# Kernel optimization log

Hardware: AMD Instinct MI355X
Metric: run time of the kernel (lower is better)

The kernel has to match this reference:

```python
import jax, jax.numpy as jnp
import numpy as np
from jax import lax

B, FQ, T, H = 2, 257, 100, 96
S, DIN, N, R, KF, KM = 8, 192, 16, 6, 5, 4
GROUPS = 8

def _ln(x, g, b, eps=1e-5):
    m = x.mean(-1, keepdims=True)
    v = ((x - m) ** 2).mean(-1, keepdims=True)
    return (x - m) / jnp.sqrt(v + eps) * g + b

def _silu(x):
    return x * jax.nn.sigmoid(x)

def _fconv(x, g, b, cw, cb, alpha):
    Bb, Fq, Tt, Hh = x.shape
    y = _ln(x, g, b)  # LayerNorm over hidden dim H (seq_last=True path)
    y = y.transpose(0, 2, 3, 1).reshape(Bb * Tt, Hh, Fq)
    pad = (cw.shape[-1] - 1) // 2
    y = lax.conv_general_dilated(y, cw, (1,), [(pad, pad)],
                                 feature_group_count=GROUPS,
                                 dimension_numbers=('NCH', 'OIH', 'NCH')) + cb[:, None]
    y = jnp.where(y > 0, y, alpha[:, None] * y)  # PReLU per channel
    return y.reshape(Bb, Tt, Hh, Fq).transpose(0, 3, 1, 2)

def _full(x, g, b, sq_w, sq_b, fw, fb, uw, ub):
    Bb, Fq, Tt, Hh = x.shape
    y = _ln(x, g, b).transpose(0, 2, 3, 1).reshape(Bb * Tt, Hh, Fq)
    y = _silu(jnp.einsum('bhf,sh->bsf', y, sq_w) + sq_b[:, None])   # squeeze 1x1 conv
    y = jnp.einsum('bgf,gkf->bgk', y, fw) + fb                      # grouped full-band linear
    y = _silu(jnp.einsum('bsf,hs->bhf', y, uw) + ub[:, None])       # unsqueeze 1x1 conv
    return y.reshape(Bb, Tt, Hh, Fq).transpose(0, 3, 1, 2)

def _mamba(x, in_w, cw, cb, xp_w, dt_w, dt_b, A_log, Dp, out_w):
    # x: [Bm, T, H] -> Mamba selective scan (d_inner=DIN, d_state=N, dt_rank=R)
    Bm, Tt, Hh = x.shape
    xz = x @ in_w.T                                  # [Bm,T,2*DIN]
    xin, z = xz[..., :DIN], xz[..., DIN:]
    xc = xin.transpose(0, 2, 1)                      # [Bm,DIN,T]
    xc = lax.conv_general_dilated(xc, cw, (1,), [(KM - 1, 0)],
                                  feature_group_count=DIN,
                                  dimension_numbers=('NCH', 'OIH', 'NCH')) + cb[:, None]
    xc = _silu(xc).transpose(0, 2, 1)                # [Bm,T,DIN]
    dbl = xc @ xp_w.T                                # [Bm,T,R+2N]
    dt = jax.nn.softplus(dbl[..., :R] @ dt_w.T + dt_b)
    Bs, Cs = dbl[..., R:R + N], dbl[..., R + N:R + 2 * N]
    A = -jnp.exp(A_log)                              # [DIN,N]

    def step(h, inp):
        dt_t, x_t, B_t, C_t = inp
        h = jnp.exp(dt_t[..., None] * A) * h + (dt_t * x_t)[..., None] * B_t[:, None, :]
        return h, jnp.einsum('bdn,bn->bd', h, C_t)

    h0 = jnp.zeros((Bm, DIN, N), x.dtype)
    _, ys = lax.scan(step, h0, (dt.transpose(1, 0, 2), xc.transpose(1, 0, 2),
                                Bs.transpose(1, 0, 2), Cs.transpose(1, 0, 2)))
    y = ys.transpose(1, 0, 2) + xc * Dp
    return (y * _silu(z)) @ out_w.T

def setup_inputs():
    key = jax.random.key(0)
    ks = jax.random.split(key, 32)
    n = lambda i, shape, s=0.1: jax.random.normal(ks[i], shape) * s
    inp = dict(
        x=jax.random.normal(ks[0], (B, FQ, T, H)),
        ln1_g=jnp.ones((H,)), ln1_b=jnp.zeros((H,)),
        conv1_w=n(1, (H, H // GROUPS, KF), 0.2), conv1_b=n(2, (H,)),
        prelu1_a=jnp.full((H,), 0.25),
        lnf_g=jnp.ones((H,)), lnf_b=jnp.zeros((H,)),
        sq_w=n(3, (S, H)), sq_b=n(4, (S,)),
        full_w=n(5, (S, FQ, FQ), 0.06), full_b=n(6, (S, FQ)),
        unsq_w=n(7, (H, S), 0.3), unsq_b=n(8, (H,)),
        ln2_g=jnp.ones((H,)), ln2_b=jnp.zeros((H,)),
        conv2_w=n(9, (H, H // GROUPS, KF), 0.2), conv2_b=n(10, (H,)),
        prelu2_a=jnp.full((H,), 0.25),
        lnm_g=jnp.ones((H,)), lnm_b=jnp.zeros((H,)),
    )
    for p, off in (('m0_', 11), ('m1_', 21)):
        inp[p + 'in_w'] = n(off, (2 * DIN, H))
        inp[p + 'conv_w'] = n(off + 1, (DIN, 1, KM), 0.3)
        inp[p + 'conv_b'] = n(off + 2, (DIN,))
        inp[p + 'xp_w'] = n(off + 3, (R + 2 * N, DIN))
        inp[p + 'dt_w'] = n(off + 4, (DIN, R))
        inp[p + 'dt_b'] = n(off + 5, (DIN,)) - 2.0
        inp[p + 'A_log'] = jnp.log(jax.random.uniform(ks[off + 6], (DIN, N), minval=0.5, maxval=1.5))
        inp[p + 'D'] = jnp.ones((DIN,)) + n(off + 7, (DIN,))
        inp[p + 'out_w'] = n(off + 8, (H, DIN))
    return inp

def reference(x, ln1_g, ln1_b, conv1_w, conv1_b, prelu1_a,
              lnf_g, lnf_b, sq_w, sq_b, full_w, full_b, unsq_w, unsq_b,
              ln2_g, ln2_b, conv2_w, conv2_b, prelu2_a, lnm_g, lnm_b,
              m0_in_w, m0_conv_w, m0_conv_b, m0_xp_w, m0_dt_w, m0_dt_b, m0_A_log, m0_D, m0_out_w,
              m1_in_w, m1_conv_w, m1_conv_b, m1_xp_w, m1_dt_w, m1_dt_b, m1_A_log, m1_D, m1_out_w):
    x = x + _fconv(x, ln1_g, ln1_b, conv1_w, conv1_b, prelu1_a)
    x = x + _full(x, lnf_g, lnf_b, sq_w, sq_b, full_w, full_b, unsq_w, unsq_b)
    x = x + _fconv(x, ln2_g, ln2_b, conv2_w, conv2_b, prelu2_a)
    Bb, Fq, Tt, Hh = x.shape
    xn = _ln(x, lnm_g, lnm_b)
    yf = _mamba(xn.reshape(Bb * Fq, Tt, Hh),
                m0_in_w, m0_conv_w, m0_conv_b, m0_xp_w, m0_dt_w, m0_dt_b, m0_A_log, m0_D, m0_out_w)
    yb = _mamba(jnp.flip(xn, 2).reshape(Bb * Fq, Tt, Hh),
                m1_in_w, m1_conv_w, m1_conv_b, m1_xp_w, m1_dt_w, m1_dt_b, m1_A_log, m1_D, m1_out_w)
    x_fw = x + yf.reshape(Bb, Fq, Tt, Hh)
    x_bw = jnp.flip(x, 2) + yb.reshape(Bb, Fq, Tt, Hh)
    return (x_fw + jnp.flip(x_bw, 2)) / 2
```

## Files before the change

### kernel.cpp

```cpp
#include <hip/hip_runtime.h>
#include <math.h>

constexpr int kB   = 2;
constexpr int kF   = 257;
constexpr int kT   = 100;
constexpr int kH   = 96;
constexpr int kS   = 8;
constexpr int kD   = 192;
constexpr int kN   = 16;
constexpr int kR   = 6;
constexpr int kKF  = 5;
constexpr int kKM  = 4;
constexpr int kG   = 8;
constexpr int kGC  = kH / kG;
constexpr int kBM  = kB * kF;
constexpr int kROWS = kB * kF * kT;
constexpr int kNX  = kROWS * kH;
constexpr int kNM  = kROWS * kD;
constexpr int kDBL = kR + 2 * kN;
constexpr int kDBLP = 48;

__device__ inline float wave_reduce_sum(float v) {
    for (int o = 32; o > 0; o >>= 1) v += __shfl_xor(v, o, 64);
    return v;
}
__device__ inline float silu_f(float x) { return x / (1.f + __expf(-x)); }
__device__ inline float softplus_f(float x) { return x > 20.f ? x : log1pf(__expf(x)); }

__global__ void ln_kernel(const float* __restrict__ in, float* __restrict__ out,
                          const float* __restrict__ g, const float* __restrict__ b,
                          int rows) {
    int wave = threadIdx.x >> 6;
    int lane = threadIdx.x & 63;
    int r = blockIdx.x * 4 + wave;
    if (r >= rows) return;
    const float* p = in + (size_t)r * kH;
    float v0 = p[lane];
    float v1 = (lane < 32) ? p[64 + lane] : 0.f;
    float s = wave_reduce_sum(v0 + v1);
    float mean = s * (1.f / 96.f);
    float d0 = v0 - mean;
    float d1 = (lane < 32) ? (v1 - mean) : 0.f;
    float vs = wave_reduce_sum(d0 * d0 + d1 * d1);
    float rstd = rsqrtf(vs * (1.f / 96.f) + 1e-5f);
    float* q = out + (size_t)r * kH;
    q[lane] = d0 * rstd * g[lane] + b[lane];
    if (lane < 32) q[64 + lane] = d1 * rstd * g[64 + lane] + b[64 + lane];
}

#define FDOT(S,K) \
  acc += xw[S][0].x*wr[K][0] + xw[S][0].y*wr[K][1] + xw[S][0].z*wr[K][2] + xw[S][0].w*wr[K][3] \
       + xw[S][1].x*wr[K][4] + xw[S][1].y*wr[K][5] + xw[S][1].z*wr[K][6] + xw[S][1].w*wr[K][7] \
       + xw[S][2].x*wr[K][8] + xw[S][2].y*wr[K][9] + xw[S][2].z*wr[K][10]+ xw[S][2].w*wr[K][11];

#define FSTEP(S0,S1,S2,S3,S4)                                              \
  if (f < fmax) {                                                          \
    const float4* cp = (const float4*)(Xs + (f + 4) * 12);                 \
    xw[S4][0] = cp[0]; xw[S4][1] = cp[1]; xw[S4][2] = cp[2];               \
    float acc = bias;                                                      \
    FDOT(S0,0) FDOT(S1,1) FDOT(S2,2) FDOT(S3,3) FDOT(S4,4)                 \
    float yv = acc > 0.f ? acc : alpha_h * acc;                            \
    size_t oi = ((size_t)(bb * kF + f) * kT + tt) * kH + g12 + hh;         \
    out[oi] = resid[oi] + yv;                                              \
    f++;                                                                   \
  }

__global__ __launch_bounds__(256)
void fconv_kernel(const float* __restrict__ ln, const float* __restrict__ resid,
                  float* __restrict__ out, const float* __restrict__ w,
                  const float* __restrict__ cb, const float* __restrict__ alpha) {
    __shared__ float Xs[261 * 12];
    __shared__ float Ws[kGC * kKF * 12];
    int g = blockIdx.x, tt = blockIdx.y, bb = blockIdx.z;
    int g12 = g * 12;
    int tid = threadIdx.x;

    for (int i = tid; i < 720; i += 256) Ws[i] = w[g * 720 + i];
    for (int i = tid; i < 257 * 12; i += 256) {
        int fs = i / 12, ci = i - fs * 12;
        Xs[(fs + 2) * 12 + ci] = ln[((size_t)(bb * kF + fs) * kT + tt) * kH + g12 + ci];
    }
    if (tid < 48) {
        const int padr[4] = {0, 1, 259, 260};
        Xs[padr[tid / 12] * 12 + (tid % 12)] = 0.f;
    }
    __syncthreads();

    int lane = tid & 63, wave = tid >> 6;
    int hh = lane % 12, fi = lane / 12;
    if (fi >= 5) return;
    int slot = wave * 5 + fi;
    int f0 = slot * 13;
    int fmax = min(f0 + 13, kF);

    float wr[5][12];
    #pragma unroll
    for (int k = 0; k < 5; k++)
        #pragma unroll
        for (int ci = 0; ci < 12; ci++)
            wr[k][ci] = Ws[hh * 60 + ci * 5 + k];

    float bias = cb[g12 + hh];
    float alpha_h = alpha[g12 + hh];

    float4 xw[5][3];
    #pragma unroll
    for (int s = 0; s < 4; s++) {
        int row = min(f0 + s, 260);
        const float4* cp = (const float4*)(Xs + row * 12);
        xw[s][0] = cp[0]; xw[s][1] = cp[1]; xw[s][2] = cp[2];
    }
    int f = f0;
    for (int rep = 0; rep < 3; rep++) {
        FSTEP(0,1,2,3,4)
        FSTEP(1,2,3,4,0)
        FSTEP(2,3,4,0,1)
        FSTEP(3,4,0,1,2)
        FSTEP(4,0,1,2,3)
    }
}

__global__ void squeeze_kernel(const float* __restrict__ ln, float* __restrict__ s1,
                               const float* __restrict__ sqw, const float* __restrict__ sqb) {
    int bt = blockIdx.x;
    int f = blockIdx.y * 64 + threadIdx.x;
    if (f >= kF) return;
    int b = bt / kT, t = bt % kT;
    const float* row = ln + ((size_t)(b * kF + f) * kT + t) * kH;
    float acc[kS];
    for (int s = 0; s < kS; s++) acc[s] = 0.f;
    for (int h = 0; h < kH; h++) {
        float v = row[h];
        for (int s = 0; s < kS; s++) acc[s] += v * sqw[s * kH + h];
    }
    for (int s = 0; s < kS; s++)
        s1[((size_t)bt * kS + s) * kF + f] = silu_f(acc[s] + sqb[s]);
}

__global__ __launch_bounds__(256)
void fullmat_gemm(const float* __restrict__ s1, float* __restrict__ s2,
                  const float* __restrict__ fw, const float* __restrict__ fb) {
    __shared__ float As[64 * 64];
    __shared__ float Bs[64 * 64];
    int k0 = blockIdx.x * 64, bt0 = blockIdx.y * 64, g = blockIdx.z;
    int tid = threadIdx.x;
    int rt = tid >> 4, ct = tid & 15;
    float acc[4][4];
    #pragma unroll
    for (int i = 0; i < 4; i++)
        #pragma unroll
        for (int j = 0; j < 4; j++) acc[i][j] = 0.f;

    for (int f0 = 0; f0 < kF; f0 += 64) {
        int fcnt = min(64, kF - f0);
        for (int i = tid; i < 64 * 64; i += 256) {
            int m = i & 63, fk = i >> 6;
            int bt = bt0 + m, f = f0 + fk;
            As[fk * 64 + m] = (bt < kB * kT && f < kF)
                ? s1[((size_t)bt * kS + g) * kF + f] : 0.f;
            int k = k0 + m;
            Bs[fk * 64 + m] = (k < kF && f < kF)
                ? fw[(size_t)g * kF * kF + (size_t)k * kF + f] : 0.f;
        }
        __syncthreads();
        for (int f = 0; f < fcnt; f++) {
            float4 a4 = *(const float4*)&As[f * 64 + rt * 4];
            float4 b4 = *(const float4*)&Bs[f * 64 + ct * 4];
            float ar[4] = {a4.x, a4.y, a4.z, a4.w};
            float br[4] = {b4.x, b4.y, b4.z, b4.w};
            #pragma unroll
            for (int i = 0; i < 4; i++)
                #pragma unroll
                for (int j = 0; j < 4; j++) acc[i][j] += ar[i] * br[j];
        }
        __syncthreads();
    }
    #pragma unroll
    for (int i = 0; i < 4; i++) {
        int bt = bt0 + rt * 4 + i;
        if (bt >= kB * kT) continue;
        #pragma unroll
        for (int j = 0; j < 4; j++) {
            int k = k0 + ct * 4 + j;
            if (k >= kF) continue;
            s2[((size_t)bt * kS + g) * kF + k] = acc[i][j] + fb[g * kF + k];
        }
    }
}

__global__ void unsqueeze_kernel(const float* __restrict__ s2, float* __restrict__ x,
                                 const float* __restrict__ uw, const float* __restrict__ ub) {
    int idx = blockIdx.x * blockDim.x + threadIdx.x;
    if (idx >= kNX) return;
    int h = idx % kH;
    int t = (idx / kH) % kT;
    int f = (idx / (kH * kT)) % kF;
    int b = idx / (kH * kT * kF);
    int bt = b * kT + t;
    float acc = ub[h];
    for (int s = 0; s < kS; s++)
        acc += s2[((size_t)bt * kS + s) * kF + f] * uw[h * kS + s];
    x[idx] += silu_f(acc);
}

__global__ void transpose_kernel(const float* __restrict__ in, float* __restrict__ out,
                                 int rows, int cols) {
    int idx = blockIdx.x * blockDim.x + threadIdx.x;
    if (idx >= rows * cols) return;
    int r = idx / cols, c = idx % cols;
    out[c * rows + r] = in[idx];
}

__global__ void xppad_kernel(const float* __restrict__ w, float* __restrict__ wp) {
    int i = blockIdx.x * 256 + threadIdx.x;
    if (i >= kD * kDBLP) return;
    int d = i / kDBLP, n = i % kDBLP;
    wp[i] = (n < kDBL) ? w[n * kD + d] : 0.f;
}

__global__ __launch_bounds__(256)
void inproj_gemm(const float* __restrict__ xn, const float* __restrict__ wT,
                 float* __restrict__ xin, float* __restrict__ z) {
    __shared__ float Al[64 * 96];
    int r0 = blockIdx.x * 64;
    int c0 = blockIdx.y * 128;
    int tid = threadIdx.x;
    for (int i = tid; i < 64 * 24; i += 256) {
        int rr = i / 24, cq = i - rr * 24;
        int r = r0 + rr; if (r >= kROWS) r = kROWS - 1;
        *(float4*)&Al[rr * 96 + cq * 4] = *(const float4*)&xn[(size_t)r * kH + cq * 4];
    }
    __syncthreads();
    int rt = tid >> 5, ct = tid & 31;
    const float* ap = Al + rt * 8 * 96;
    const float* bp = wT + c0 + ct * 4;
    float4 acc[8];
    #pragma unroll
    for (int i = 0; i < 8; i++) acc[i] = make_float4(0.f, 0.f, 0.f, 0.f);
    for (int h = 0; h < 96; h++) {
        float4 b = *(const float4*)&bp[(size_t)h * 384];
        #pragma unroll
        for (int i = 0; i < 8; i++) {
            float av = ap[i * 96 + h];
            acc[i].x += av * b.x; acc[i].y += av * b.y;
            acc[i].z += av * b.z; acc[i].w += av * b.w;
        }
    }
    int cbase = c0 + ct * 4;
    #pragma unroll
    for (int i = 0; i < 8; i++) {
        int r = r0 + rt * 8 + i;
        if (r >= kROWS) break;
        if (cbase < kD) *(float4*)&xin[(size_t)r * kD + cbase] = acc[i];
        else            *(float4*)&z[(size_t)r * kD + cbase - kD] = acc[i];
    }
}

__global__ __launch_bounds__(256)
void outproj_gemm(const float* __restrict__ ym, const float* __restrict__ zg,
                  const float* __restrict__ wpT,
                  const float* __restrict__ xres, float* __restrict__ out, int dir) {
    __shared__ float Al[64 * 192];
    int r0 = blockIdx.x * 64;
    int tid = threadIdx.x;
    for (int i = tid; i < 64 * 48; i += 256) {
        int rr = i / 48, cq = i - rr * 48;
        int r = r0 + rr; if (r >= kROWS) r = kROWS - 1;
        size_t gidx = (size_t)r * kD + cq * 4;
        float4 a = *(const float4*)&ym[gidx];
        float4 g4 = *(const float4*)&zg[gidx];
        a.x *= silu_f(g4.x); a.y *= silu_f(g4.y);
        a.z *= silu_f(g4.z); a.w *= silu_f(g4.w);
        *(float4*)&Al[rr * 192 + cq * 4] = a;
    }
    __syncthreads();
    int rt = tid >> 5, ct = tid & 31;
    const float* ap = Al + rt * 8 * 192;
    const float* bp = wpT + ct * 3;
    float acc[8][3];
    #pragma unroll
    for (int i = 0; i < 8; i++) { acc[i][0] = 0.f; acc[i][1] = 0.f; acc[i][2] = 0.f; }
    for (int h = 0; h < 192; h++) {
        float b0 = bp[h * 96], b1 = bp[h * 96 + 1], b2 = bp[h * 96 + 2];
        #pragma unroll
        for (int i = 0; i < 8; i++) {
            float av = ap[i * 192 + h];
            acc[i][0] += av * b0; acc[i][1] += av * b1; acc[i][2] += av * b2;
        }
    }
    int cbase = ct * 3;
    #pragma unroll
    for (int i = 0; i < 8; i++) {
        int r = r0 + rt * 8 + i;
        if (r >= kROWS) break;
        size_t o = (size_t)r * kH + cbase;
        #pragma unroll
        for (int j = 0; j < 3; j++) {
            float base = dir ? out[o + j] : xres[o + j];
            out[o + j] = base + 0.5f * acc[i][j];
        }
    }
}

__global__ void mconv_kernel(const float* __restrict__ xin, float* __restrict__ xc,
                             const float* __restrict__ cw, const float* __restrict__ cb, int dir) {
    int qid = blockIdx.x * blockDim.x + threadIdx.x;
    if (qid >= kROWS * 48) return;
    int r = qid / 48, d4 = (qid - r * 48) * 4;
    int bm = r / kT, t = r - bm * kT;
    float4 acc = make_float4(cb[d4], cb[d4 + 1], cb[d4 + 2], cb[d4 + 3]);
    #pragma unroll
    for (int k = 0; k < kKM; k++) {
        int ts = dir ? (t + 3 - k) : (t + k - 3);
        if (ts < 0 || ts >= kT) continue;
        float4 v = *(const float4*)&xin[((size_t)bm * kT + ts) * kD + d4];
        acc.x += v.x * cw[(d4 + 0) * kKM + k];
        acc.y += v.y * cw[(d4 + 1) * kKM + k];
        acc.z += v.z * cw[(d4 + 2) * kKM + k];
        acc.w += v.w * cw[(d4 + 3) * kKM + k];
    }
    float4 o = make_float4(silu_f(acc.x), silu_f(acc.y), silu_f(acc.z), silu_f(acc.w));
    *(float4*)&xc[(size_t)r * kD + d4] = o;
}

__global__ __launch_bounds__(256)
void xpproj_gemm(const float* __restrict__ xc, float* __restrict__ dbl,
                 const float* __restrict__ wpx) {
    __shared__ float Al[64 * 192];
    int r0 = blockIdx.x * 64;
    int tid = threadIdx.x;
    for (int i = tid; i < 64 * 48; i += 256) {
        int rr = i / 48, cq = i - rr * 48;
        int r = r0 + rr; if (r >= kROWS) r = kROWS - 1;
        *(float4*)&Al[rr * 192 + cq * 4] = *(const float4*)&xc[(size_t)r * kD + cq * 4];
    }
    __syncthreads();
    int rt = tid >> 5, ct = tid & 31;
    if (ct >= 24) return;
    const float* ap = Al + rt * 8 * 192;
    const float* bp = wpx + ct * 2;
    float acc[8][2];
    #pragma unroll
    for (int i = 0; i < 8; i++) { acc[i][0] = 0.f; acc[i][1] = 0.f; }
    for (int h = 0; h < 192; h++) {
        float b0 = bp[h * kDBLP], b1 = bp[h * kDBLP + 1];
        #pragma unroll
        for (int i = 0; i < 8; i++) {
            float av = ap[i * 192 + h];
            acc[i][0] += av * b0; acc[i][1] += av * b1;
        }
    }
    int cbase = ct * 2;
    #pragma unroll
    for (int i = 0; i < 8; i++) {
        int r = r0 + rt * 8 + i;
        if (r >= kROWS) break;
        #pragma unroll
        for (int j = 0; j < 2; j++) {
            int c = cbase + j;
            if (c < kDBL) dbl[(size_t)r * kDBL + c] = acc[i][j];
        }
    }
}

__global__ __launch_bounds__(192)
void scan2_kernel(const float* __restrict__ dbl0, const float* __restrict__ dbl1,
                  float* __restrict__ xc0, float* __restrict__ xc1,
                  const float* __restrict__ Al0, const float* __restrict__ Al1,
                  const float* __restrict__ dtw0, const float* __restrict__ dtw1,
                  const float* __restrict__ dtb0, const float* __restrict__ dtb1,
                  const float* __restrict__ Dp0, const float* __restrict__ Dp1,
                  int dirbase) {
    __shared__ float dsg[kT * 40];
    int dd = blockIdx.y;
    int dir = dirbase + dd;
    const float* dbl   = dd ? dbl1 : dbl0;
    float* xcy         = dd ? xc1  : xc0;
    const float* A_log = dd ? Al1  : Al0;
    const float* dtw   = dd ? dtw1 : dtw0;
    const float* dtb   = dd ? dtb1 : dtb0;
    const float* Dp    = dd ? Dp1  : Dp0;

    int bm = blockIdx.x;
    int d = threadIdx.x;

    const float* drow = dbl + (size_t)bm * kT * kDBL;
    for (int i = d; i < kT * kDBL; i += 192) {
        int t = i / kDBL, j = i - t * kDBL;
        int slot = (j < 6) ? j : (j + 2);
        dsg[t * 40 + slot] = drow[i];
    }
    __syncthreads();

    float A[kN], h[kN], dw[kR];
    #pragma unroll
    for (int n = 0; n < kN; n++) { A[n] = -__expf(A_log[d * kN + n]); h[n] = 0.f; }
    #pragma unroll
    for (int j = 0; j < kR; j++) dw[j] = dtw[d * kR + j];
    float db = dtb[d], Dv = Dp[d];

    float* xrow = xcy + (size_t)bm * kT * kD + d;

    for (int tb = 0; tb < kT; tb += 4) {
        int ts[4];
        float xv[4];
        #pragma unroll
        for (int u = 0; u < 4; u++) {
            ts[u] = dir ? (kT - 1 - (tb + u)) : (tb + u);
            xv[u] = xrow[(size_t)ts[u] * kD];
        }
        #pragma unroll
        for (int u = 0; u < 4; u++) {
            const float* row = dsg + ts[u] * 40;
            float4 q0 = *(const float4*)(row);
            float4 q1 = *(const float4*)(row + 4);
            float s = db + q0.x * dw[0] + q0.y * dw[1] + q0.z * dw[2]
                         + q0.w * dw[3] + q1.x * dw[4] + q1.y * dw[5];
            float dt = softplus_f(s);
            float dtx = dt * xv[u];
            float4 B0 = *(const float4*)(row + 8);
            float4 B1 = *(const float4*)(row + 12);
            float4 B2 = *(const float4*)(row + 16);
            float4 B3 = *(const float4*)(row + 20);
            float4 C0 = *(const float4*)(row + 24);
            float4 C1 = *(const float4*)(row + 28);
            float4 C2 = *(const float4*)(row + 32);
            float4 C3 = *(const float4*)(row + 36);
            float y = 0.f;
            h[0]  = __expf(dt * A[0])  * h[0]  + dtx * B0.x;  y += h[0]  * C0.x;
            h[1]  = __expf(dt * A[1])  * h[1]  + dtx * B0.y;  y += h[1]  * C0.y;
            h[2]  = __expf(dt * A[2])  * h[2]  + dtx * B0.z;  y += h[2]  * C0.z;
            h[3]  = __expf(dt * A[3])  * h[3]  + dtx * B0.w;  y += h[3]  * C0.w;
            h[4]  = __expf(dt * A[4])  * h[4]  + dtx * B1.x;  y += h[4]  * C1.x;
            h[5]  = __expf(dt * A[5])  * h[5]  + dtx * B1.y;  y += h[5]  * C1.y;
            h[6]  = __expf(dt * A[6])  * h[6]  + dtx * B1.z;  y += h[6]  * C1.z;
            h[7]  = __expf(dt * A[7])  * h[7]  + dtx * B1.w;  y += h[7]  * C1.w;
            h[8]  = __expf(dt * A[8])  * h[8]  + dtx * B2.x;  y += h[8]  * C2.x;
            h[9]  = __expf(dt * A[9])  * h[9]  + dtx * B2.y;  y += h[9]  * C2.y;
            h[10] = __expf(dt * A[10]) * h[10] + dtx * B2.z;  y += h[10] * C2.z;
            h[11] = __expf(dt * A[11]) * h[11] + dtx * B2.w;  y += h[11] * C2.w;
            h[12] = __expf(dt * A[12]) * h[12] + dtx * B3.x;  y += h[12] * C3.x;
            h[13] = __expf(dt * A[13]) * h[13] + dtx * B3.y;  y += h[13] * C3.y;
            h[14] = __expf(dt * A[14]) * h[14] + dtx * B3.z;  y += h[14] * C3.z;
            h[15] = __expf(dt * A[15]) * h[15] + dtx * B3.w;  y += h[15] * C3.w;
            xrow[(size_t)ts[u] * kD] = y + xv[u] * Dv;
        }
    }
}

extern "C" void kernel_launch(void* const* d_in, const int* in_sizes, int n_in,
                              void* d_out, int out_size, void* d_ws, size_t ws_size,
                              hipStream_t stream) {
    const float* x       = (const float*)d_in[0];
    const float* ln1_g   = (const float*)d_in[1];
    const float* ln1_b   = (const float*)d_in[2];
    const float* conv1_w = (const float*)d_in[3];
    const float* conv1_b = (const float*)d_in[4];
    const float* prelu1  = (const float*)d_in[5];
    const float* lnf_g   = (const float*)d_in[6];
    const float* lnf_b   = (const float*)d_in[7];
    const float* sq_w    = (const float*)d_in[8];
    const float* sq_b    = (const float*)d_in[9];
    const float* full_w  = (const float*)d_in[10];
    const float* full_b  = (const float*)d_in[11];
    const float* unsq_w  = (const float*)d_in[12];
    const float* unsq_b  = (const float*)d_in[13];
    const float* ln2_g   = (const float*)d_in[14];
    const float* ln2_b   = (const float*)d_in[15];
    const float* conv2_w = (const float*)d_in[16];
    const float* conv2_b = (const float*)d_in[17];
    const float* prelu2  = (const float*)d_in[18];
    const float* lnm_g   = (const float*)d_in[19];
    const float* lnm_b   = (const float*)d_in[20];

    float* ws   = (float*)d_ws;
    float* xbuf = ws;
    float* xn   = ws + (size_t)kNX;
    float* R1   = xn + (size_t)kNX;
    float* R2   = R1 + (size_t)kNM;
    float* R3   = R2 + (size_t)kNM;
    float* wTs  = R3 + (size_t)kNM;
    float* in_wT[2]  = { wTs, wTs + 2 * kD * kH };
    float* out_wp[2] = { wTs + 2 * (2 * kD * kH),
                         wTs + 2 * (2 * kD * kH) + kD * kH };
    float* xp_wp[2]  = { wTs + 2 * (2 * kD * kH) + 2 * kD * kH,
                         wTs + 2 * (2 * kD * kH) + 2 * kD * kH + kD * kDBLP };
    float* wEnd = wTs + 2 * (2 * kD * kH) + 2 * kD * kH + 2 * kD * kDBLP;
    float* R4 = wEnd;
    float* R5 = R4 + (size_t)kNM;
    size_t need_batched = (size_t)((R5 + (size_t)kNM) - ws) * sizeof(float);
    bool batched = (ws_size >= need_batched);

    const float* mw[2][8];
    for (int dir = 0; dir < 2; dir++) {
        int wi = 21 + dir * 9;
        mw[dir][0] = (const float*)d_in[wi + 1];
        mw[dir][1] = (const float*)d_in[wi + 2];
        mw[dir][2] = (const float*)d_in[wi + 4];
        mw[dir][3] = (const float*)d_in[wi + 5];
        mw[dir][4] = (const float*)d_in[wi + 6];
        mw[dir][5] = (const float*)d_in[wi + 7];
        transpose_kernel<<<(2 * kD * kH + 255) / 256, 256, 0, stream>>>(
            (const float*)d_in[wi + 0], in_wT[dir], 2 * kD, kH);
        transpose_kernel<<<(kH * kD + 255) / 256, 256, 0, stream>>>(
            (const float*)d_in[wi + 8], out_wp[dir], kH, kD);
        xppad_kernel<<<(kD * kDBLP + 255) / 256, 256, 0, stream>>>(
            (const float*)d_in[wi + 3], xp_wp[dir]);
    }

    int lnGrid = (kROWS + 3) / 4;
    int nxGrid = (kNX + 255) / 256;
    dim3 fcGrid(kG, kT, kB);
    int gemmGrid = (kROWS + 63) / 64;
    int mcGrid = (kROWS * 48 + 255) / 256;

    ln_kernel<<<lnGrid, 256, 0, stream>>>(x, R1, ln1_g, ln1_b, kROWS);
    fconv_kernel<<<fcGrid, 256, 0, stream>>>(R1, x, xbuf, conv1_w, conv1_b, prelu1);

    ln_kernel<<<lnGrid, 256, 0, stream>>>(xbuf, R1, lnf_g, lnf_b, kROWS);
    squeeze_kernel<<<dim3(kB * kT, (kF + 63) / 64), 64, 0, stream>>>(R1, R2, sq_w, sq_b);
    fullmat_gemm<<<dim3(5, 4, kS), 256, 0, stream>>>(R2, R3, full_w, full_b);
    unsqueeze_kernel<<<nxGrid, 256, 0, stream>>>(R3, xbuf, unsq_w, unsq_b);

    ln_kernel<<<lnGrid, 256, 0, stream>>>(xbuf, R1, ln2_g, ln2_b, kROWS);
    fconv_kernel<<<fcGrid, 256, 0, stream>>>(R1, xbuf, xbuf, conv2_w, conv2_b, prelu2);

    ln_kernel<<<lnGrid, 256, 0, stream>>>(xbuf, xn, lnm_g, lnm_b, kROWS);

    if (batched) {
        float* dbl0 = xn;
        float* dbl1 = xn + (size_t)kROWS * kDBL;
        inproj_gemm<<<dim3(gemmGrid, 3), 256, 0, stream>>>(xn, in_wT[0], R1, R2);
        mconv_kernel<<<mcGrid, 256, 0, stream>>>(R1, R4, mw[0][0], mw[0][1], 0);
        inproj_gemm<<<dim3(gemmGrid, 3), 256, 0, stream>>>(xn, in_wT[1], R1, R3);
        mconv_kernel<<<mcGrid, 256, 0, stream>>>(R1, R5, mw[1][0], mw[1][1], 1);
        xpproj_gemm<<<gemmGrid, 256, 0, stream>>>(R4, dbl0, xp_wp[0]);
        xpproj_gemm<<<gemmGrid, 256, 0, stream>>>(R5, dbl1, xp_wp[1]);
        scan2_kernel<<<dim3(kBM, 2), 192, 0, stream>>>(
            dbl0, dbl1, R4, R5,
            mw[0][4], mw[1][4], mw[0][2], mw[1][2],
            mw[0][3], mw[1][3], mw[0][5], mw[1][5], 0);
        outproj_gemm<<<gemmGrid, 256, 0, stream>>>(R4, R2, out_wp[0], xbuf, (float*)d_out, 0);
        outproj_gemm<<<gemmGrid, 256, 0, stream>>>(R5, R3, out_wp[1], xbuf, (float*)d_out, 1);
    } else {
        for (int dir = 0; dir < 2; dir++) {
            inproj_gemm<<<dim3(gemmGrid, 3), 256, 0, stream>>>(xn, in_wT[dir], R1, R2);
            mconv_kernel<<<mcGrid, 256, 0, stream>>>(R1, R3, mw[dir][0], mw[dir][1], dir);
            xpproj_gemm<<<gemmGrid, 256, 0, stream>>>(R3, R1, xp_wp[dir]);
            scan2_kernel<<<dim3(kBM, 1), 192, 0, stream>>>(
                R1, R1, R3, R3,
                mw[dir][4], mw[dir][4], mw[dir][2], mw[dir][2],
                mw[dir][3], mw[dir][3], mw[dir][5], mw[dir][5], dir);
            outproj_gemm<<<gemmGrid, 256, 0, stream>>>(R3, R2, out_wp[dir], xbuf, (float*)d_out, dir);
        }
    }
}
```

Measured before the change: 876.6 us.

## Fuse LayerNorm with squeeze and unsqueeze with LayerNorm; use exp2 in scan

Merges the full-band LayerNorm with the squeeze projection into one wave-per-row kernel, and merges the unsqueeze residual update with the following LayerNorm. This removes two kernel launches and several full-tensor round trips through global memory for the normalized intermediates. The selective scan now pre-scales A by log2(e) and calls exp2f instead of __expf, saving a multiply per state update. In exchange, the fused squeeze does eight wave reductions per row and writes scattered single floats from lane 0.

```diff
diff --git a/kernel.cpp b/kernel.cpp
--- a/kernel.cpp
+++ b/kernel.cpp
@@ -48,6 +48,91 @@
     if (lane < 32) q[64 + lane] = d1 * rstd * g[64 + lane] + b[64 + lane];
 }
 
+__global__ __launch_bounds__(256)
+void lnsq_kernel(const float* __restrict__ in, float* __restrict__ s1,
+                 const float* __restrict__ g, const float* __restrict__ b,
+                 const float* __restrict__ sqw, const float* __restrict__ sqb) {
+    __shared__ float sws[kS * kH];
+    int tid = threadIdx.x;
+    for (int i = tid; i < kS * kH; i += 256) sws[i] = sqw[i];
+    __syncthreads();
+    int wave = tid >> 6, lane = tid & 63;
+    int r = blockIdx.x * 4 + wave;
+    if (r >= kROWS) return;
+    int b_ = r / (kF * kT);
+    int rem = r - b_ * kF * kT;
+    int f = rem / kT;
+    int t = rem - f * kT;
+    const float* p = in + (size_t)r * kH;
+    float v0 = p[lane];
+    float v1 = (lane < 32) ? p[64 + lane] : 0.f;
+    float s = wave_reduce_sum(v0 + v1);
+    float mean = s * (1.f / 96.f);
+    float d0 = v0 - mean;
+    float d1 = (lane < 32) ? (v1 - mean) : 0.f;
+    float vs = wave_reduce_sum(d0 * d0 + d1 * d1);
+    float rstd = rsqrtf(vs * (1.f / 96.f) + 1e-5f);
+    float n0 = d0 * rstd * g[lane] + b[lane];
+    float n1 = 0.f;
+    if (lane < 32) n1 = d1 * rstd * g[64 + lane] + b[64 + lane];
+    int bt = b_ * kT + t;
+    #pragma unroll
+    for (int sq = 0; sq < kS; sq++) {
+        float part = n0 * sws[sq * kH + lane]
+                   + ((lane < 32) ? n1 * sws[sq * kH + 64 + lane] : 0.f);
+        part = wave_reduce_sum(part);
+        if (lane == 0)
+            s1[((size_t)bt * kS + sq) * kF + f] = silu_f(part + sqb[sq]);
+    }
+}
+
+__global__ __launch_bounds__(256)
+void unsq_ln_kernel(const float* __restrict__ s2, float* __restrict__ x,
+                    const float* __restrict__ uw, const float* __restrict__ ub,
+                    const float* __restrict__ g2, const float* __restrict__ b2,
+                    float* __restrict__ lnout) {
+    __shared__ float uws[kH * kS];
+    int tid = threadIdx.x;
+    for (int i = tid; i < kH * kS; i += 256) uws[i] = uw[i];
+    __syncthreads();
+    int wave = tid >> 6, lane = tid & 63;
+    int r = blockIdx.x * 4 + wave;
+    if (r >= kROWS) return;
+    int b_ = r / (kF * kT);
+    int rem = r - b_ * kF * kT;
+    int f = rem / kT;
+    int t = rem - f * kT;
+    int bt = b_ * kT + t;
+    float sv[kS];
+    #pragma unroll
+    for (int sq = 0; sq < kS; sq++)
+        sv[sq] = s2[((size_t)bt * kS + sq) * kF + f];
+    float* xr = x + (size_t)r * kH;
+    int h0 = lane, h1 = 64 + lane;
+    float acc0 = ub[h0];
+    #pragma unroll
+    for (int sq = 0; sq < kS; sq++) acc0 += sv[sq] * uws[h0 * kS + sq];
+    float x0 = xr[h0] + silu_f(acc0);
+    float x1 = 0.f;
+    if (lane < 32) {
+        float acc1 = ub[h1];
+        #pragma unroll
+        for (int sq = 0; sq < kS; sq++) acc1 += sv[sq] * uws[h1 * kS + sq];
+        x1 = xr[h1] + silu_f(acc1);
+    }
+    xr[h0] = x0;
+    if (lane < 32) xr[h1] = x1;
+    float s = wave_reduce_sum(x0 + x1);
+    float mean = s * (1.f / 96.f);
+    float d0 = x0 - mean;
+    float d1 = (lane < 32) ? (x1 - mean) : 0.f;
+    float vs = wave_reduce_sum(d0 * d0 + d1 * d1);
+    float rstd = rsqrtf(vs * (1.f / 96.f) + 1e-5f);
+    float* q = lnout + (size_t)r * kH;
+    q[h0] = d0 * rstd * g2[h0] + b2[h0];
+    if (lane < 32) q[h1] = d1 * rstd * g2[h1] + b2[h1];
+}
+
 #define FDOT(S,K) \
   acc += xw[S][0].x*wr[K][0] + xw[S][0].y*wr[K][1] + xw[S][0].z*wr[K][2] + xw[S][0].w*wr[K][3] \
        + xw[S][1].x*wr[K][4] + xw[S][1].y*wr[K][5] + xw[S][1].z*wr[K][6] + xw[S][1].w*wr[K][7] \
@@ -120,23 +205,6 @@
     }
 }
 
-__global__ void squeeze_kernel(const float* __restrict__ ln, float* __restrict__ s1,
-                               const float* __restrict__ sqw, const float* __restrict__ sqb) {
-    int bt = blockIdx.x;
-    int f = blockIdx.y * 64 + threadIdx.x;
-    if (f >= kF) return;
-    int b = bt / kT, t = bt % kT;
-    const float* row = ln + ((size_t)(b * kF + f) * kT + t) * kH;
-    float acc[kS];
-    for (int s = 0; s < kS; s++) acc[s] = 0.f;
-    for (int h = 0; h < kH; h++) {
-        float v = row[h];
-        for (int s = 0; s < kS; s++) acc[s] += v * sqw[s * kH + h];
-    }
-    for (int s = 0; s < kS; s++)
-        s1[((size_t)bt * kS + s) * kF + f] = silu_f(acc[s] + sqb[s]);
-}
-
 __global__ __launch_bounds__(256)
 void fullmat_gemm(const float* __restrict__ s1, float* __restrict__ s2,
                   const float* __restrict__ fw, const float* __restrict__ fb) {
@@ -186,21 +254,6 @@
             s2[((size_t)bt * kS + g) * kF + k] = acc[i][j] + fb[g * kF + k];
         }
     }
-}
-
-__global__ void unsqueeze_kernel(const float* __restrict__ s2, float* __restrict__ x,
-                                 const float* __restrict__ uw, const float* __restrict__ ub) {
-    int idx = blockIdx.x * blockDim.x + threadIdx.x;
-    if (idx >= kNX) return;
-    int h = idx % kH;
-    int t = (idx / kH) % kT;
-    int f = (idx / (kH * kT)) % kF;
-    int b = idx / (kH * kT * kF);
-    int bt = b * kT + t;
-    float acc = ub[h];
-    for (int s = 0; s < kS; s++)
-        acc += s2[((size_t)bt * kS + s) * kF + f] * uw[h * kS + s];
-    x[idx] += silu_f(acc);
 }
 
 __global__ void transpose_kernel(const float* __restrict__ in, float* __restrict__ out,
@@ -392,9 +445,10 @@
     }
     __syncthreads();
 
-    float A[kN], h[kN], dw[kR];
-    #pragma unroll
-    for (int n = 0; n < kN; n++) { A[n] = -__expf(A_log[d * kN + n]); h[n] = 0.f; }
+    constexpr float kLog2e = 1.44269504088896f;
+    float A2[kN], h[kN], dw[kR];
+    #pragma unroll
+    for (int n = 0; n < kN; n++) { A2[n] = -__expf(A_log[d * kN + n]) * kLog2e; h[n] = 0.f; }
     #pragma unroll
     for (int j = 0; j < kR; j++) dw[j] = dtw[d * kR + j];
     float db = dtb[d], Dv = Dp[d];
@@ -427,22 +481,22 @@
             float4 C2 = *(const float4*)(row + 32);
             float4 C3 = *(const float4*)(row + 36);
             float y = 0.f;
-            h[0]  = __expf(dt * A[0])  * h[0]  + dtx * B0.x;  y += h[0]  * C0.x;
-            h[1]  = __expf(dt * A[1])  * h[1]  + dtx * B0.y;  y += h[1]  * C0.y;
-            h[2]  = __expf(dt * A[2])  * h[2]  + dtx * B0.z;  y += h[2]  * C0.z;
-            h[3]  = __expf(dt * A[3])  * h[3]  + dtx * B0.w;  y += h[3]  * C0.w;
-            h[4]  = __expf(dt * A[4])  * h[4]  + dtx * B1.x;  y += h[4]  * C1.x;
-            h[5]  = __expf(dt * A[5])  * h[5]  + dtx * B1.y;  y += h[5]  * C1.y;
-            h[6]  = __expf(dt * A[6])  * h[6]  + dtx * B1.z;  y += h[6]  * C1.z;
-            h[7]  = __expf(dt * A[7])  * h[7]  + dtx * B1.w;  y += h[7]  * C1.w;
-            h[8]  = __expf(dt * A[8])  * h[8]  + dtx * B2.x;  y += h[8]  * C2.x;
-            h[9]  = __expf(dt * A[9])  * h[9]  + dtx * B2.y;  y += h[9]  * C2.y;
-            h[10] = __expf(dt * A[10]) * h[10] + dtx * B2.z;  y += h[10] * C2.z;
-            h[11] = __expf(dt * A[11]) * h[11] + dtx * B2.w;  y += h[11] * C2.w;
-            h[12] = __expf(dt * A[12]) * h[12] + dtx * B3.x;  y += h[12] * C3.x;
-            h[13] = __expf(dt * A[13]) * h[13] + dtx * B3.y;  y += h[13] * C3.y;
-            h[14] = __expf(dt * A[14]) * h[14] + dtx * B3.z;  y += h[14] * C3.z;
-            h[15] = __expf(dt * A[15]) * h[15] + dtx * B3.w;  y += h[15] * C3.w;
+            h[0]  = exp2f(dt * A2[0])  * h[0]  + dtx * B0.x;  y += h[0]  * C0.x;
+            h[1]  = exp2f(dt * A2[1])  * h[1]  + dtx * B0.y;  y += h[1]  * C0.y;
+            h[2]  = exp2f(dt * A2[2])  * h[2]  + dtx * B0.z;  y += h[2]  * C0.z;
+            h[3]  = exp2f(dt * A2[3])  * h[3]  + dtx * B0.w;  y += h[3]  * C0.w;
+            h[4]  = exp2f(dt * A2[4])  * h[4]  + dtx * B1.x;  y += h[4]  * C1.x;
+            h[5]  = exp2f(dt * A2[5])  * h[5]  + dtx * B1.y;  y += h[5]  * C1.y;
+            h[6]  = exp2f(dt * A2[6])  * h[6]  + dtx * B1.z;  y += h[6]  * C1.z;
+            h[7]  = exp2f(dt * A2[7])  * h[7]  + dtx * B1.w;  y += h[7]  * C1.w;
+            h[8]  = exp2f(dt * A2[8])  * h[8]  + dtx * B2.x;  y += h[8]  * C2.x;
+            h[9]  = exp2f(dt * A2[9])  * h[9]  + dtx * B2.y;  y += h[9]  * C2.y;
+            h[10] = exp2f(dt * A2[10]) * h[10] + dtx * B2.z;  y += h[10] * C2.z;
+            h[11] = exp2f(dt * A2[11]) * h[11] + dtx * B2.w;  y += h[11] * C2.w;
+            h[12] = exp2f(dt * A2[12]) * h[12] + dtx * B3.x;  y += h[12] * C3.x;
+            h[13] = exp2f(dt * A2[13]) * h[13] + dtx * B3.y;  y += h[13] * C3.y;
+            h[14] = exp2f(dt * A2[14]) * h[14] + dtx * B3.z;  y += h[14] * C3.z;
+            h[15] = exp2f(dt * A2[15]) * h[15] + dtx * B3.w;  y += h[15] * C3.w;
             xrow[(size_t)ts[u] * kD] = y + xv[u] * Dv;
         }
     }
@@ -509,7 +563,6 @@
     }
 
     int lnGrid = (kROWS + 3) / 4;
-    int nxGrid = (kNX + 255) / 256;
     dim3 fcGrid(kG, kT, kB);
     int gemmGrid = (kROWS + 63) / 64;
     int mcGrid = (kROWS * 48 + 255) / 256;
@@ -517,12 +570,10 @@
     ln_kernel<<<lnGrid, 256, 0, stream>>>(x, R1, ln1_g, ln1_b, kROWS);
     fconv_kernel<<<fcGrid, 256, 0, stream>>>(R1, x, xbuf, conv1_w, conv1_b, prelu1);
 
-    ln_kernel<<<lnGrid, 256, 0, stream>>>(xbuf, R1, lnf_g, lnf_b, kROWS);
-    squeeze_kernel<<<dim3(kB * kT, (kF + 63) / 64), 64, 0, stream>>>(R1, R2, sq_w, sq_b);
+    lnsq_kernel<<<lnGrid, 256, 0, stream>>>(xbuf, R2, lnf_g, lnf_b, sq_w, sq_b);
     fullmat_gemm<<<dim3(5, 4, kS), 256, 0, stream>>>(R2, R3, full_w, full_b);
-    unsqueeze_kernel<<<nxGrid, 256, 0, stream>>>(R3, xbuf, unsq_w, unsq_b);
-
-    ln_kernel<<<lnGrid, 256, 0, stream>>>(xbuf, R1, ln2_g, ln2_b, kROWS);
+    unsq_ln_kernel<<<lnGrid, 256, 0, stream>>>(R3, xbuf, unsq_w, unsq_b, ln2_g, ln2_b, R1);
+
     fconv_kernel<<<fcGrid, 256, 0, stream>>>(R1, xbuf, xbuf, conv2_w, conv2_b, prelu2);
 
     ln_kernel<<<lnGrid, 256, 0, stream>>>(xbuf, xn, lnm_g, lnm_b, kROWS);
```

Measured after the change: 922.9 us. 5.3% more time.
